# Kernel optimization log

Hardware: AMD Instinct MI355X
Metric: run time of the kernel (lower is better)

The kernel has to match this reference:

```python
import jax, jax.numpy as jnp
import numpy as np

C = 256
H_CH = 128  # channels // 2 (stage_index != 2)


def _gelu(x):
    # torch nn.GELU() default: exact erf formulation
    return jax.nn.gelu(x, approximate=False)


def _ln_channels(x, gamma, beta):
    # LayerNorm over channel dim (axis=1) of NCHW, eps=1e-5 (torch default)
    mu = jnp.mean(x, axis=1, keepdims=True)
    var = jnp.var(x, axis=1, keepdims=True)
    xn = (x - mu) * jax.lax.rsqrt(var + 1e-5)
    return xn * gamma[None, :, None, None] + beta[None, :, None, None]


def setup_inputs() -> dict:
    key = jax.random.key(0)
    ks = jax.random.split(key, 9)
    x = jax.random.normal(ks[0], (16, C, 64, 64), dtype=jnp.float32)
    s1 = 1.0 / np.sqrt(C)
    s2 = 1.0 / np.sqrt(H_CH)
    W1 = jax.random.uniform(ks[1], (H_CH, C), jnp.float32, -s1, s1)
    b1 = jax.random.uniform(ks[2], (H_CH,), jnp.float32, -s1, s1)
    g1 = jnp.ones((H_CH,), jnp.float32)
    be1 = jnp.zeros((H_CH,), jnp.float32)
    W2 = jax.random.uniform(ks[3], (C, H_CH), jnp.float32, -s2, s2)
    b2 = jax.random.uniform(ks[4], (C,), jnp.float32, -s2, s2)
    g2 = jnp.ones((C,), jnp.float32)
    be2 = jnp.zeros((C,), jnp.float32)
    return {"x": x, "W1": W1, "b1": b1, "g1": g1, "be1": be1,
            "W2": W2, "b2": b2, "g2": g2, "be2": be2}


def reference(x, W1, b1, g1, be1, W2, b2, g2, be2):
    identity = x
    # 1x1 conv == per-pixel channel matmul
    h = jnp.einsum('bchw,oc->bohw', x, W1) + b1[None, :, None, None]
    h = _gelu(_ln_channels(h, g1, be1))
    y = jnp.einsum('bchw,oc->bohw', h, W2) + b2[None, :, None, None]
    y = _ln_channels(y, g2, be2)
    return _gelu(y + identity)
```

## Files before the change

kernel.cpp:

```cpp
#include <hip/hip_runtime.h>

#define C_IN 256
#define HC   128
#define HW   4096
#define TP   64

#define SX 260
#define SH 132
#define SO 68

typedef __attribute__((ext_vector_type(8))) short short8;
typedef __attribute__((ext_vector_type(4))) short short4v;
typedef __attribute__((ext_vector_type(4))) float f32x4;
typedef __attribute__((ext_vector_type(2))) float f32x2;
typedef __attribute__((ext_vector_type(4))) unsigned short u16x4;

__device__ __forceinline__ unsigned short f2bf(float f) {
    union { float f; unsigned int u; } v; v.f = f;
    return (unsigned short)((v.u + 0x7FFFu + ((v.u >> 16) & 1u)) >> 16);
}

__device__ __forceinline__ float gelu_f(float v) {
    const float u = v * (0.7978845608028654f + 0.035677408136300125f * v * v);
    const float e = exp2f(u * 2.8853900817779268f);
    const float t = 1.0f - 2.0f * __builtin_amdgcn_rcpf(e + 1.0f);
    return 0.5f * v * (1.0f + t);
}

__device__ __forceinline__ void block_sync() {
    asm volatile("s_waitcnt lgkmcnt(0)" ::: "memory");
    __builtin_amdgcn_s_barrier();
    asm volatile("" ::: "memory");
    __builtin_amdgcn_sched_barrier(0);
}

__device__ __forceinline__ void wave_lds_fence() {
    asm volatile("s_waitcnt lgkmcnt(0)" ::: "memory");
}

__global__ void convert_weights(const float* __restrict__ W1, const float* __restrict__ W2,
                                unsigned short* __restrict__ W1b, unsigned short* __restrict__ W2b) {
    int i = blockIdx.x * blockDim.x + threadIdx.x;
    if (i < HC * C_IN) { W1b[i] = f2bf(W1[i]); W2b[i] = f2bf(W2[i]); }
}

union SmemU {
    unsigned short Xs[TP * SX];
    struct { unsigned short Hs[TP * SH]; float Ob[4][16][SO]; } u2;
};

template<bool USE_WS>
__global__ __launch_bounds__(256, 4) void fused_mlp(
    const float* __restrict__ x,
    const float* __restrict__ W1, const float* __restrict__ b1,
    const float* __restrict__ g1, const float* __restrict__ be1,
    const float* __restrict__ W2, const float* __restrict__ b2,
    const float* __restrict__ g2, const float* __restrict__ be2,
    const unsigned short* __restrict__ W1b, const unsigned short* __restrict__ W2b,
    float* __restrict__ out)
{
    __shared__ alignas(16) SmemU sm;
    __shared__ float red[4][TP][2];

    const int tid = threadIdx.x;
    const int wv  = tid >> 6;
    const int l   = tid & 63;
    const int l15 = l & 15;
    const int kg  = l >> 4;

    const int bid = blockIdx.x;
    const int b   = bid >> 6;
    const int p0  = (bid & 63) * TP;
    const float* xb = x   + (size_t)b * (C_IN * HW) + p0;
    float*       ob = out + (size_t)b * (C_IN * HW) + p0;

    const int g  = l15;
    const int cs = wv * 16 + kg * 4;
    f32x4 v0[8], v1[8];
    #pragma unroll
    for (int rnd = 0; rnd < 2; ++rnd)
        #pragma unroll
        for (int j = 0; j < 4; ++j)
            v0[rnd * 4 + j] = *reinterpret_cast<const f32x4*>(xb + (size_t)(rnd * 64 + cs + j) * HW + g * 4);
    #pragma unroll
    for (int rnd = 0; rnd < 2; ++rnd)
        #pragma unroll
        for (int j = 0; j < 4; ++j)
            v1[rnd * 4 + j] = *reinterpret_cast<const f32x4*>(xb + (size_t)((rnd + 2) * 64 + cs + j) * HW + g * 4);
    #pragma unroll
    for (int rnd = 0; rnd < 2; ++rnd) {
        const int c0 = rnd * 64 + cs;
        #pragma unroll
        for (int jj = 0; jj < 4; ++jj) {
            u16x4 pk;
            #pragma unroll
            for (int j = 0; j < 4; ++j) pk[j] = f2bf(v0[rnd * 4 + j][jj]);
            *reinterpret_cast<u16x4*>(&sm.Xs[(size_t)(g * 4 + jj) * SX + c0]) = pk;
        }
    }
    block_sync();

    f32x4 acc1[2][4];
    const f32x4 vzero = {0.f, 0.f, 0.f, 0.f};
    #pragma unroll
    for (int mt = 0; mt < 2; ++mt)
        #pragma unroll
        for (int nt = 0; nt < 4; ++nt) acc1[mt][nt] = vzero;

    const int r0 = wv * 32;
    #pragma unroll
    for (int ks = 0; ks < 4; ++ks) {
        const int kb = ks * 32 + kg * 8;
        short8 a[2]; short4v blo[4], bhi[4];
        #pragma unroll
        for (int mt = 0; mt < 2; ++mt) {
            const int row = r0 + mt * 16 + l15;
            if constexpr (USE_WS) {
                a[mt] = *reinterpret_cast<const short8*>(W1b + (size_t)row * C_IN + kb);
            } else {
                const float* wp = W1 + (size_t)row * C_IN + kb;
                const f32x4 f0 = *reinterpret_cast<const f32x4*>(wp);
                const f32x4 f1 = *reinterpret_cast<const f32x4*>(wp + 4);
                #pragma unroll
                for (int e = 0; e < 4; ++e) { a[mt][e] = (short)f2bf(f0[e]); a[mt][4+e] = (short)f2bf(f1[e]); }
            }
        }
        #pragma unroll
        for (int nt = 0; nt < 4; ++nt) {
            const unsigned short* p = &sm.Xs[(size_t)(nt * 16 + l15) * SX + kb];
            blo[nt] = *reinterpret_cast<const short4v*>(p);
            bhi[nt] = *reinterpret_cast<const short4v*>(p + 4);
        }
        #pragma unroll
        for (int mt = 0; mt < 2; ++mt)
            #pragma unroll
            for (int nt = 0; nt < 4; ++nt) {
                const short8 bf = __builtin_shufflevector(blo[nt], bhi[nt], 0,1,2,3,4,5,6,7);
                acc1[mt][nt] = __builtin_amdgcn_mfma_f32_16x16x32_bf16(a[mt], bf, acc1[mt][nt], 0, 0, 0);
            }
    }

    #pragma unroll
    for (int rnd = 0; rnd < 2; ++rnd) {
        const int c0 = (rnd + 2) * 64 + cs;
        #pragma unroll
        for (int jj = 0; jj < 4; ++jj) {
            u16x4 pk;
            #pragma unroll
            for (int j = 0; j < 4; ++j) pk[j] = f2bf(v1[rnd * 4 + j][jj]);
            *reinterpret_cast<u16x4*>(&sm.Xs[(size_t)(g * 4 + jj) * SX + c0]) = pk;
        }
    }
    block_sync();

    #pragma unroll
    for (int ks = 4; ks < 8; ++ks) {
        const int kb = ks * 32 + kg * 8;
        short8 a[2]; short4v blo[4], bhi[4];
        #pragma unroll
        for (int mt = 0; mt < 2; ++mt) {
            const int row = r0 + mt * 16 + l15;
            if constexpr (USE_WS) {
                a[mt] = *reinterpret_cast<const short8*>(W1b + (size_t)row * C_IN + kb);
            } else {
                const float* wp = W1 + (size_t)row * C_IN + kb;
                const f32x4 f0 = *reinterpret_cast<const f32x4*>(wp);
                const f32x4 f1 = *reinterpret_cast<const f32x4*>(wp + 4);
                #pragma unroll
                for (int e = 0; e < 4; ++e) { a[mt][e] = (short)f2bf(f0[e]); a[mt][4+e] = (short)f2bf(f1[e]); }
            }
        }
        #pragma unroll
        for (int nt = 0; nt < 4; ++nt) {
            const unsigned short* p = &sm.Xs[(size_t)(nt * 16 + l15) * SX + kb];
            blo[nt] = *reinterpret_cast<const short4v*>(p);
            bhi[nt] = *reinterpret_cast<const short4v*>(p + 4);
        }
        #pragma unroll
        for (int mt = 0; mt < 2; ++mt)
            #pragma unroll
            for (int nt = 0; nt < 4; ++nt) {
                const short8 bf = __builtin_shufflevector(blo[nt], bhi[nt], 0,1,2,3,4,5,6,7);
                acc1[mt][nt] = __builtin_amdgcn_mfma_f32_16x16x32_bf16(a[mt], bf, acc1[mt][nt], 0, 0, 0);
            }
    }

    #pragma unroll
    for (int mt = 0; mt < 2; ++mt) {
        const f32x4 bias = *reinterpret_cast<const f32x4*>(b1 + r0 + mt * 16 + kg * 4);
        #pragma unroll
        for (int nt = 0; nt < 4; ++nt) acc1[mt][nt] += bias;
    }
    #pragma unroll
    for (int nt = 0; nt < 4; ++nt) {
        float s = 0.f, q = 0.f;
        #pragma unroll
        for (int mt = 0; mt < 2; ++mt)
            #pragma unroll
            for (int r = 0; r < 4; ++r) { const float v = acc1[mt][nt][r]; s += v; q += v * v; }
        s += __shfl_xor(s, 16); s += __shfl_xor(s, 32);
        q += __shfl_xor(q, 16); q += __shfl_xor(q, 32);
        if (kg == 0) { red[wv][nt * 16 + l15][0] = s; red[wv][nt * 16 + l15][1] = q; }
    }
    block_sync();

    {
        f32x4 gm[2], bt[2];
        #pragma unroll
        for (int mt = 0; mt < 2; ++mt) {
            gm[mt] = *reinterpret_cast<const f32x4*>(g1  + r0 + mt * 16 + kg * 4);
            bt[mt] = *reinterpret_cast<const f32x4*>(be1 + r0 + mt * 16 + kg * 4);
        }
        #pragma unroll
        for (int nt = 0; nt < 4; ++nt) {
            const int col = nt * 16 + l15;
            float s = 0.f, q = 0.f;
            #pragma unroll
            for (int w2 = 0; w2 < 4; ++w2) { s += red[w2][col][0]; q += red[w2][col][1]; }
            const float mean = s * (1.0f / HC);
            const float rstd = rsqrtf(q * (1.0f / HC) - mean * mean + 1e-5f);
            #pragma unroll
            for (int mt = 0; mt < 2; ++mt) {
                u16x4 pk;
                #pragma unroll
                for (int r = 0; r < 4; ++r) {
                    float v = (acc1[mt][nt][r] - mean) * rstd;
                    v = v * gm[mt][r] + bt[mt][r];
                    pk[r] = f2bf(gelu_f(v));
                }
                *reinterpret_cast<u16x4*>(&sm.u2.Hs[(size_t)col * SH + r0 + mt * 16 + kg * 4]) = pk;
            }
        }
    }
    block_sync();

    const int r2 = wv * 64;
    f32x4 xp[4];
    #pragma unroll
    for (int m = 0; m < 4; ++m)
        xp[m] = *reinterpret_cast<const f32x4*>(xb + (size_t)(r2 + kg + 4 * m) * HW + l15 * 4);

    f32x4 acc2[4][4];
    #pragma unroll
    for (int mt = 0; mt < 4; ++mt)
        #pragma unroll
        for (int nt = 0; nt < 4; ++nt) acc2[mt][nt] = vzero;

    #pragma unroll
    for (int ks = 0; ks < 4; ++ks) {
        const int kb = ks * 32 + kg * 8;
        short4v blo[4], bhi[4];
        #pragma unroll
        for (int nt = 0; nt < 4; ++nt) {
            const unsigned short* p = &sm.u2.Hs[(size_t)(nt * 16 + l15) * SH + kb];
            blo[nt] = *reinterpret_cast<const short4v*>(p);
            bhi[nt] = *reinterpret_cast<const short4v*>(p + 4);
        }
        #pragma unroll
        for (int half = 0; half < 2; ++half) {
            short8 a[2];
            #pragma unroll
            for (int m2 = 0; m2 < 2; ++m2) {
                const int row = r2 + (half * 2 + m2) * 16 + l15;
                if constexpr (USE_WS) {
                    a[m2] = *reinterpret_cast<const short8*>(W2b + (size_t)row * HC + kb);
                } else {
                    const float* wp = W2 + (size_t)row * HC + kb;
                    const f32x4 f0 = *reinterpret_cast<const f32x4*>(wp);
                    const f32x4 f1 = *reinterpret_cast<const f32x4*>(wp + 4);
                    #pragma unroll
                    for (int e = 0; e < 4; ++e) { a[m2][e] = (short)f2bf(f0[e]); a[m2][4+e] = (short)f2bf(f1[e]); }
                }
            }
            #pragma unroll
            for (int m2 = 0; m2 < 2; ++m2)
                #pragma unroll
                for (int nt = 0; nt < 4; ++nt) {
                    const short8 bf = __builtin_shufflevector(blo[nt], bhi[nt], 0,1,2,3,4,5,6,7);
                    acc2[half * 2 + m2][nt] = __builtin_amdgcn_mfma_f32_16x16x32_bf16(a[m2], bf, acc2[half * 2 + m2][nt], 0, 0, 0);
                }
        }
    }

    #pragma unroll
    for (int mt = 0; mt < 4; ++mt) {
        const f32x4 bias = *reinterpret_cast<const f32x4*>(b2 + r2 + mt * 16 + kg * 4);
        #pragma unroll
        for (int nt = 0; nt < 4; ++nt) acc2[mt][nt] += bias;
    }
    #pragma unroll
    for (int nt = 0; nt < 4; ++nt) {
        float s = 0.f, q = 0.f;
        #pragma unroll
        for (int mt = 0; mt < 4; ++mt)
            #pragma unroll
            for (int r = 0; r < 4; ++r) { const float v = acc2[mt][nt][r]; s += v; q += v * v; }
        s += __shfl_xor(s, 16); s += __shfl_xor(s, 32);
        q += __shfl_xor(q, 16); q += __shfl_xor(q, 32);
        if (kg == 0) { red[wv][nt * 16 + l15][0] = s; red[wv][nt * 16 + l15][1] = q; }
    }
    block_sync();

    float mean2[4], rstd2[4];
    #pragma unroll
    for (int nt = 0; nt < 4; ++nt) {
        const int col = nt * 16 + l15;
        float s = 0.f, q = 0.f;
        #pragma unroll
        for (int w2 = 0; w2 < 4; ++w2) { s += red[w2][col][0]; q += red[w2][col][1]; }
        mean2[nt] = s * (1.0f / C_IN);
        rstd2[nt] = rsqrtf(q * (1.0f / C_IN) - mean2[nt] * mean2[nt] + 1e-5f);
    }

    #pragma unroll
    for (int mt = 0; mt < 4; ++mt) {
        const f32x4 gm = *reinterpret_cast<const f32x4*>(g2  + r2 + mt * 16 + kg * 4);
        const f32x4 bt = *reinterpret_cast<const f32x4*>(be2 + r2 + mt * 16 + kg * 4);
        #pragma unroll
        for (int nt = 0; nt < 4; ++nt) {
            #pragma unroll
            for (int r = 0; r < 4; ++r) {
                float v = (acc2[mt][nt][r] - mean2[nt]) * rstd2[nt];
                v = v * gm[r] + bt[r];
                sm.u2.Ob[wv][kg * 4 + r][nt * 16 + l15] = v;
            }
        }
        f32x4 xn[4];
        if (mt < 3) {
            #pragma unroll
            for (int m = 0; m < 4; ++m)
                xn[m] = *reinterpret_cast<const f32x4*>(xb + (size_t)(r2 + (mt + 1) * 16 + kg + 4 * m) * HW + l15 * 4);
        }
        wave_lds_fence();
        #pragma unroll
        for (int m = 0; m < 4; ++m) {
            const int rl  = kg + 4 * m;
            const int row = r2 + mt * 16 + rl;
            const float* op = &sm.u2.Ob[wv][rl][l15 * 4];
            const f32x2 ylo = *reinterpret_cast<const f32x2*>(op);
            const f32x2 yhi = *reinterpret_cast<const f32x2*>(op + 2);
            f32x4 o4;
            o4[0] = gelu_f(ylo[0] + xp[m][0]);
            o4[1] = gelu_f(ylo[1] + xp[m][1]);
            o4[2] = gelu_f(yhi[0] + xp[m][2]);
            o4[3] = gelu_f(yhi[1] + xp[m][3]);
            *reinterpret_cast<f32x4*>(ob + (size_t)row * HW + l15 * 4) = o4;
        }
        #pragma unroll
        for (int m = 0; m < 4; ++m) xp[m] = xn[m];
        if (mt < 3) wave_lds_fence();
    }
}

extern "C" void kernel_launch(void* const* d_in, const int* in_sizes, int n_in,
                              void* d_out, int out_size, void* d_ws, size_t ws_size,
                              hipStream_t stream) {
    const float* x   = (const float*)d_in[0];
    const float* W1  = (const float*)d_in[1];
    const float* b1  = (const float*)d_in[2];
    const float* g1  = (const float*)d_in[3];
    const float* be1 = (const float*)d_in[4];
    const float* W2  = (const float*)d_in[5];
    const float* b2  = (const float*)d_in[6];
    const float* g2  = (const float*)d_in[7];
    const float* be2 = (const float*)d_in[8];
    float* out = (float*)d_out;

    const size_t need = (size_t)(HC * C_IN + C_IN * HC) * sizeof(unsigned short);
    if (ws_size >= need) {
        unsigned short* W1b = (unsigned short*)d_ws;
        unsigned short* W2b = W1b + HC * C_IN;
        convert_weights<<<128, 256, 0, stream>>>(W1, W2, W1b, W2b);
        fused_mlp<true><<<1024, 256, 0, stream>>>(x, W1, b1, g1, be1, W2, b2, g2, be2, W1b, W2b, out);
    } else {
        fused_mlp<false><<<1024, 256, 0, stream>>>(x, W1, b1, g1, be1, W2, b2, g2, be2, nullptr, nullptr, out);
    }
}
```

Before: 57.97 us.

## Split X staging by pixel halves and overlap second-half conversion with GEMM1

The X tile is now loaded as two pixel halves instead of two channel halves, each spanning all 256 channels. The first GEMM runs over the full K on the first 32 pixels, and the bf16 conversion and LDS stores of the second 32 pixels are spread across its k-steps. The second pixel half is then processed over the full K. This is meant to hide the conversion and store work behind MFMA execution and to change the global load pattern to 128-byte pixel runs. In exchange, W1 A-fragments are loaded twice, once for each pixel half, and each k-step issues fewer MFMAs.

```diff
diff --git a/kernel.cpp b/kernel.cpp
--- a/kernel.cpp
+++ b/kernel.cpp
@@ -74,28 +74,30 @@
     const float* xb = x   + (size_t)b * (C_IN * HW) + p0;
     float*       ob = out + (size_t)b * (C_IN * HW) + p0;
 
-    const int g  = l15;
-    const int cs = wv * 16 + kg * 4;
-    f32x4 v0[8], v1[8];
+    const int gs = tid & 7;
+    const int cq = tid >> 3;
+
+    f32x4 vA[8], vB[8];
     #pragma unroll
     for (int rnd = 0; rnd < 2; ++rnd)
         #pragma unroll
         for (int j = 0; j < 4; ++j)
-            v0[rnd * 4 + j] = *reinterpret_cast<const f32x4*>(xb + (size_t)(rnd * 64 + cs + j) * HW + g * 4);
+            vA[rnd * 4 + j] = *reinterpret_cast<const f32x4*>(xb + (size_t)(rnd * 128 + cq * 4 + j) * HW + gs * 4);
     #pragma unroll
     for (int rnd = 0; rnd < 2; ++rnd)
         #pragma unroll
         for (int j = 0; j < 4; ++j)
-            v1[rnd * 4 + j] = *reinterpret_cast<const f32x4*>(xb + (size_t)((rnd + 2) * 64 + cs + j) * HW + g * 4);
+            vB[rnd * 4 + j] = *reinterpret_cast<const f32x4*>(xb + (size_t)(rnd * 128 + cq * 4 + j) * HW + 32 + gs * 4);
+
     #pragma unroll
     for (int rnd = 0; rnd < 2; ++rnd) {
-        const int c0 = rnd * 64 + cs;
+        const int c0 = rnd * 128 + cq * 4;
         #pragma unroll
         for (int jj = 0; jj < 4; ++jj) {
             u16x4 pk;
             #pragma unroll
-            for (int j = 0; j < 4; ++j) pk[j] = f2bf(v0[rnd * 4 + j][jj]);
-            *reinterpret_cast<u16x4*>(&sm.Xs[(size_t)(g * 4 + jj) * SX + c0]) = pk;
+            for (int j = 0; j < 4; ++j) pk[j] = f2bf(vA[rnd * 4 + j][jj]);
+            *reinterpret_cast<u16x4*>(&sm.Xs[(size_t)(gs * 4 + jj) * SX + c0]) = pk;
         }
     }
     block_sync();
@@ -109,9 +111,9 @@
 
     const int r0 = wv * 32;
     #pragma unroll
-    for (int ks = 0; ks < 4; ++ks) {
+    for (int ks = 0; ks < 8; ++ks) {
         const int kb = ks * 32 + kg * 8;
-        short8 a[2]; short4v blo[4], bhi[4];
+        short8 a[2]; short4v blo[2], bhi[2];
         #pragma unroll
         for (int mt = 0; mt < 2; ++mt) {
             const int row = r0 + mt * 16 + l15;
@@ -126,7 +128,7 @@
             }
         }
         #pragma unroll
-        for (int nt = 0; nt < 4; ++nt) {
+        for (int nt = 0; nt < 2; ++nt) {
             const unsigned short* p = &sm.Xs[(size_t)(nt * 16 + l15) * SX + kb];
             blo[nt] = *reinterpret_cast<const short4v*>(p);
             bhi[nt] = *reinterpret_cast<const short4v*>(p + 4);
@@ -134,29 +136,24 @@
         #pragma unroll
         for (int mt = 0; mt < 2; ++mt)
             #pragma unroll
-            for (int nt = 0; nt < 4; ++nt) {
+            for (int nt = 0; nt < 2; ++nt) {
                 const short8 bf = __builtin_shufflevector(blo[nt], bhi[nt], 0,1,2,3,4,5,6,7);
                 acc1[mt][nt] = __builtin_amdgcn_mfma_f32_16x16x32_bf16(a[mt], bf, acc1[mt][nt], 0, 0, 0);
             }
-    }
-
-    #pragma unroll
-    for (int rnd = 0; rnd < 2; ++rnd) {
-        const int c0 = (rnd + 2) * 64 + cs;
-        #pragma unroll
-        for (int jj = 0; jj < 4; ++jj) {
+        {
+            const int rnd = ks >> 2, jj = ks & 3;
             u16x4 pk;
             #pragma unroll
-            for (int j = 0; j < 4; ++j) pk[j] = f2bf(v1[rnd * 4 + j][jj]);
-            *reinterpret_cast<u16x4*>(&sm.Xs[(size_t)(g * 4 + jj) * SX + c0]) = pk;
-        }
-    }
-    block_sync();
-
-    #pragma unroll
-    for (int ks = 4; ks < 8; ++ks) {
+            for (int j = 0; j < 4; ++j) pk[j] = f2bf(vB[rnd * 4 + j][jj]);
+            *reinterpret_cast<u16x4*>(&sm.Xs[(size_t)(32 + gs * 4 + jj) * SX + rnd * 128 + cq * 4]) = pk;
+        }
+    }
+    block_sync();
+
+    #pragma unroll
+    for (int ks = 0; ks < 8; ++ks) {
         const int kb = ks * 32 + kg * 8;
-        short8 a[2]; short4v blo[4], bhi[4];
+        short8 a[2]; short4v blo[2], bhi[2];
         #pragma unroll
         for (int mt = 0; mt < 2; ++mt) {
             const int row = r0 + mt * 16 + l15;
@@ -171,17 +168,17 @@
             }
         }
         #pragma unroll
-        for (int nt = 0; nt < 4; ++nt) {
-            const unsigned short* p = &sm.Xs[(size_t)(nt * 16 + l15) * SX + kb];
+        for (int nt = 0; nt < 2; ++nt) {
+            const unsigned short* p = &sm.Xs[(size_t)((nt + 2) * 16 + l15) * SX + kb];
             blo[nt] = *reinterpret_cast<const short4v*>(p);
             bhi[nt] = *reinterpret_cast<const short4v*>(p + 4);
         }
         #pragma unroll
         for (int mt = 0; mt < 2; ++mt)
             #pragma unroll
-            for (int nt = 0; nt < 4; ++nt) {
+            for (int nt = 0; nt < 2; ++nt) {
                 const short8 bf = __builtin_shufflevector(blo[nt], bhi[nt], 0,1,2,3,4,5,6,7);
-                acc1[mt][nt] = __builtin_amdgcn_mfma_f32_16x16x32_bf16(a[mt], bf, acc1[mt][nt], 0, 0, 0);
+                acc1[mt][nt + 2] = __builtin_amdgcn_mfma_f32_16x16x32_bf16(a[mt], bf, acc1[mt][nt + 2], 0, 0, 0);
             }
     }
 
```

New measurement: 62.66 us. +8.1%, slower.

## Process two pixel tiles per block and prefetch the next tile's input during GEMM2

Applied to the files above, without the earlier changes.

Each block now handles two consecutive 64-pixel tiles, launching half as many blocks. The second tile's x data is loaded into registers after the first tile's LayerNorm-1, so the load overlaps GEMM2 and the epilogue. Shared memory is doubled to two buffers, and launch bounds drop to 2 blocks per CU. This targets exposed global load latency at the cost of lower occupancy, more register pressure, and fewer blocks to fill the GPU.

```diff
diff --git a/kernel.cpp b/kernel.cpp
--- a/kernel.cpp
+++ b/kernel.cpp
@@ -50,7 +50,7 @@
 };
 
 template<bool USE_WS>
-__global__ __launch_bounds__(256, 4) void fused_mlp(
+__global__ __launch_bounds__(256, 2) void fused_mlp(
     const float* __restrict__ x,
     const float* __restrict__ W1, const float* __restrict__ b1,
     const float* __restrict__ g1, const float* __restrict__ be1,
@@ -59,7 +59,7 @@
     const unsigned short* __restrict__ W1b, const unsigned short* __restrict__ W2b,
     float* __restrict__ out)
 {
-    __shared__ alignas(16) SmemU sm;
+    __shared__ alignas(16) SmemU sm[2];
     __shared__ float red[4][TP][2];
 
     const int tid = threadIdx.x;
@@ -68,287 +68,254 @@
     const int l15 = l & 15;
     const int kg  = l >> 4;
 
-    const int bid = blockIdx.x;
-    const int b   = bid >> 6;
-    const int p0  = (bid & 63) * TP;
-    const float* xb = x   + (size_t)b * (C_IN * HW) + p0;
-    float*       ob = out + (size_t)b * (C_IN * HW) + p0;
-
     const int g  = l15;
     const int cs = wv * 16 + kg * 4;
-    f32x4 v0[8], v1[8];
+
+    const int r0 = wv * 32;
+    const int r2 = wv * 64;
+    const f32x4 vzero = {0.f, 0.f, 0.f, 0.f};
+
+    const int tile0 = blockIdx.x * 2;
+    const float* xb0 = x + (size_t)(tile0 >> 6) * (C_IN * HW) + (tile0 & 63) * TP;
+    f32x4 vA[16];
     #pragma unroll
-    for (int rnd = 0; rnd < 2; ++rnd)
+    for (int rnd = 0; rnd < 4; ++rnd)
         #pragma unroll
         for (int j = 0; j < 4; ++j)
-            v0[rnd * 4 + j] = *reinterpret_cast<const f32x4*>(xb + (size_t)(rnd * 64 + cs + j) * HW + g * 4);
+            vA[rnd * 4 + j] = *reinterpret_cast<const f32x4*>(xb0 + (size_t)(rnd * 64 + cs + j) * HW + g * 4);
+
     #pragma unroll
-    for (int rnd = 0; rnd < 2; ++rnd)
-        #pragma unroll
-        for (int j = 0; j < 4; ++j)
-            v1[rnd * 4 + j] = *reinterpret_cast<const f32x4*>(xb + (size_t)((rnd + 2) * 64 + cs + j) * HW + g * 4);
-    #pragma unroll
-    for (int rnd = 0; rnd < 2; ++rnd) {
-        const int c0 = rnd * 64 + cs;
-        #pragma unroll
-        for (int jj = 0; jj < 4; ++jj) {
-            u16x4 pk;
-            #pragma unroll
-            for (int j = 0; j < 4; ++j) pk[j] = f2bf(v0[rnd * 4 + j][jj]);
-            *reinterpret_cast<u16x4*>(&sm.Xs[(size_t)(g * 4 + jj) * SX + c0]) = pk;
-        }
-    }
-    block_sync();
-
-    f32x4 acc1[2][4];
-    const f32x4 vzero = {0.f, 0.f, 0.f, 0.f};
-    #pragma unroll
-    for (int mt = 0; mt < 2; ++mt)
-        #pragma unroll
-        for (int nt = 0; nt < 4; ++nt) acc1[mt][nt] = vzero;
-
-    const int r0 = wv * 32;
-    #pragma unroll
-    for (int ks = 0; ks < 4; ++ks) {
-        const int kb = ks * 32 + kg * 8;
-        short8 a[2]; short4v blo[4], bhi[4];
+    for (int t = 0; t < 2; ++t) {
+        SmemU& S = sm[t];
+        const int tile = blockIdx.x * 2 + t;
+        const float* xb = x   + (size_t)(tile >> 6) * (C_IN * HW) + (tile & 63) * TP;
+        float*       ob = out + (size_t)(tile >> 6) * (C_IN * HW) + (tile & 63) * TP;
+
+        #pragma unroll
+        for (int rnd = 0; rnd < 4; ++rnd) {
+            const int c0 = rnd * 64 + cs;
+            #pragma unroll
+            for (int jj = 0; jj < 4; ++jj) {
+                u16x4 pk;
+                #pragma unroll
+                for (int j = 0; j < 4; ++j) pk[j] = f2bf(vA[rnd * 4 + j][jj]);
+                *reinterpret_cast<u16x4*>(&S.Xs[(size_t)(g * 4 + jj) * SX + c0]) = pk;
+            }
+        }
+        block_sync();
+
+        f32x4 acc1[2][4];
+        #pragma unroll
+        for (int mt = 0; mt < 2; ++mt)
+            #pragma unroll
+            for (int nt = 0; nt < 4; ++nt) acc1[mt][nt] = vzero;
+
+        #pragma unroll
+        for (int ks = 0; ks < 8; ++ks) {
+            const int kb = ks * 32 + kg * 8;
+            short8 a[2]; short4v blo[4], bhi[4];
+            #pragma unroll
+            for (int mt = 0; mt < 2; ++mt) {
+                const int row = r0 + mt * 16 + l15;
+                if constexpr (USE_WS) {
+                    a[mt] = *reinterpret_cast<const short8*>(W1b + (size_t)row * C_IN + kb);
+                } else {
+                    const float* wp = W1 + (size_t)row * C_IN + kb;
+                    const f32x4 f0 = *reinterpret_cast<const f32x4*>(wp);
+                    const f32x4 f1 = *reinterpret_cast<const f32x4*>(wp + 4);
+                    #pragma unroll
+                    for (int e = 0; e < 4; ++e) { a[mt][e] = (short)f2bf(f0[e]); a[mt][4+e] = (short)f2bf(f1[e]); }
+                }
+            }
+            #pragma unroll
+            for (int nt = 0; nt < 4; ++nt) {
+                const unsigned short* p = &S.Xs[(size_t)(nt * 16 + l15) * SX + kb];
+                blo[nt] = *reinterpret_cast<const short4v*>(p);
+                bhi[nt] = *reinterpret_cast<const short4v*>(p + 4);
+            }
+            #pragma unroll
+            for (int mt = 0; mt < 2; ++mt)
+                #pragma unroll
+                for (int nt = 0; nt < 4; ++nt) {
+                    const short8 bf = __builtin_shufflevector(blo[nt], bhi[nt], 0,1,2,3,4,5,6,7);
+                    acc1[mt][nt] = __builtin_amdgcn_mfma_f32_16x16x32_bf16(a[mt], bf, acc1[mt][nt], 0, 0, 0);
+                }
+        }
+
         #pragma unroll
         for (int mt = 0; mt < 2; ++mt) {
-            const int row = r0 + mt * 16 + l15;
-            if constexpr (USE_WS) {
-                a[mt] = *reinterpret_cast<const short8*>(W1b + (size_t)row * C_IN + kb);
-            } else {
-                const float* wp = W1 + (size_t)row * C_IN + kb;
-                const f32x4 f0 = *reinterpret_cast<const f32x4*>(wp);
-                const f32x4 f1 = *reinterpret_cast<const f32x4*>(wp + 4);
-                #pragma unroll
-                for (int e = 0; e < 4; ++e) { a[mt][e] = (short)f2bf(f0[e]); a[mt][4+e] = (short)f2bf(f1[e]); }
-            }
+            const f32x4 bias = *reinterpret_cast<const f32x4*>(b1 + r0 + mt * 16 + kg * 4);
+            #pragma unroll
+            for (int nt = 0; nt < 4; ++nt) acc1[mt][nt] += bias;
         }
         #pragma unroll
         for (int nt = 0; nt < 4; ++nt) {
-            const unsigned short* p = &sm.Xs[(size_t)(nt * 16 + l15) * SX + kb];
-            blo[nt] = *reinterpret_cast<const short4v*>(p);
-            bhi[nt] = *reinterpret_cast<const short4v*>(p + 4);
-        }
-        #pragma unroll
-        for (int mt = 0; mt < 2; ++mt)
+            float s = 0.f, q = 0.f;
+            #pragma unroll
+            for (int mt = 0; mt < 2; ++mt)
+                #pragma unroll
+                for (int r = 0; r < 4; ++r) { const float v = acc1[mt][nt][r]; s += v; q += v * v; }
+            s += __shfl_xor(s, 16); s += __shfl_xor(s, 32);
+            q += __shfl_xor(q, 16); q += __shfl_xor(q, 32);
+            if (kg == 0) { red[wv][nt * 16 + l15][0] = s; red[wv][nt * 16 + l15][1] = q; }
+        }
+        block_sync();
+
+        {
+            f32x4 gm[2], bt[2];
+            #pragma unroll
+            for (int mt = 0; mt < 2; ++mt) {
+                gm[mt] = *reinterpret_cast<const f32x4*>(g1  + r0 + mt * 16 + kg * 4);
+                bt[mt] = *reinterpret_cast<const f32x4*>(be1 + r0 + mt * 16 + kg * 4);
+            }
             #pragma unroll
             for (int nt = 0; nt < 4; ++nt) {
-                const short8 bf = __builtin_shufflevector(blo[nt], bhi[nt], 0,1,2,3,4,5,6,7);
-                acc1[mt][nt] = __builtin_amdgcn_mfma_f32_16x16x32_bf16(a[mt], bf, acc1[mt][nt], 0, 0, 0);
-            }
-    }
-
-    #pragma unroll
-    for (int rnd = 0; rnd < 2; ++rnd) {
-        const int c0 = (rnd + 2) * 64 + cs;
-        #pragma unroll
-        for (int jj = 0; jj < 4; ++jj) {
-            u16x4 pk;
-            #pragma unroll
-            for (int j = 0; j < 4; ++j) pk[j] = f2bf(v1[rnd * 4 + j][jj]);
-            *reinterpret_cast<u16x4*>(&sm.Xs[(size_t)(g * 4 + jj) * SX + c0]) = pk;
-        }
-    }
-    block_sync();
-
-    #pragma unroll
-    for (int ks = 4; ks < 8; ++ks) {
-        const int kb = ks * 32 + kg * 8;
-        short8 a[2]; short4v blo[4], bhi[4];
-        #pragma unroll
-        for (int mt = 0; mt < 2; ++mt) {
-            const int row = r0 + mt * 16 + l15;
-            if constexpr (USE_WS) {
-                a[mt] = *reinterpret_cast<const short8*>(W1b + (size_t)row * C_IN + kb);
-            } else {
-                const float* wp = W1 + (size_t)row * C_IN + kb;
-                const f32x4 f0 = *reinterpret_cast<const f32x4*>(wp);
-                const f32x4 f1 = *reinterpret_cast<const f32x4*>(wp + 4);
-                #pragma unroll
-                for (int e = 0; e < 4; ++e) { a[mt][e] = (short)f2bf(f0[e]); a[mt][4+e] = (short)f2bf(f1[e]); }
-            }
+                const int col = nt * 16 + l15;
+                float s = 0.f, q = 0.f;
+                #pragma unroll
+                for (int w2 = 0; w2 < 4; ++w2) { s += red[w2][col][0]; q += red[w2][col][1]; }
+                const float mean = s * (1.0f / HC);
+                const float rstd = rsqrtf(q * (1.0f / HC) - mean * mean + 1e-5f);
+                #pragma unroll
+                for (int mt = 0; mt < 2; ++mt) {
+                    u16x4 pk;
+                    #pragma unroll
+                    for (int r = 0; r < 4; ++r) {
+                        float v = (acc1[mt][nt][r] - mean) * rstd;
+                        v = v * gm[mt][r] + bt[mt][r];
+                        pk[r] = f2bf(gelu_f(v));
+                    }
+                    *reinterpret_cast<u16x4*>(&S.u2.Hs[(size_t)col * SH + r0 + mt * 16 + kg * 4]) = pk;
+                }
+            }
+        }
+        block_sync();
+
+        if (t == 0) {
+            const int tile1 = blockIdx.x * 2 + 1;
+            const float* xb1 = x + (size_t)(tile1 >> 6) * (C_IN * HW) + (tile1 & 63) * TP;
+            #pragma unroll
+            for (int rnd = 0; rnd < 4; ++rnd)
+                #pragma unroll
+                for (int j = 0; j < 4; ++j)
+                    vA[rnd * 4 + j] = *reinterpret_cast<const f32x4*>(xb1 + (size_t)(rnd * 64 + cs + j) * HW + g * 4);
+        }
+
+        f32x4 xp[4];
+        #pragma unroll
+        for (int m = 0; m < 4; ++m)
+            xp[m] = *reinterpret_cast<const f32x4*>(xb + (size_t)(r2 + kg + 4 * m) * HW + l15 * 4);
+
+        f32x4 acc2[4][4];
+        #pragma unroll
+        for (int mt = 0; mt < 4; ++mt)
+            #pragma unroll
+            for (int nt = 0; nt < 4; ++nt) acc2[mt][nt] = vzero;
+
+        #pragma unroll
+        for (int ks = 0; ks < 4; ++ks) {
+            const int kb = ks * 32 + kg * 8;
+            short4v blo[4], bhi[4];
+            #pragma unroll
+            for (int nt = 0; nt < 4; ++nt) {
+                const unsigned short* p = &S.u2.Hs[(size_t)(nt * 16 + l15) * SH + kb];
+                blo[nt] = *reinterpret_cast<const short4v*>(p);
+                bhi[nt] = *reinterpret_cast<const short4v*>(p + 4);
+            }
+            #pragma unroll
+            for (int half = 0; half < 2; ++half) {
+                short8 a[2];
+                #pragma unroll
+                for (int m2 = 0; m2 < 2; ++m2) {
+                    const int row = r2 + (half * 2 + m2) * 16 + l15;
+                    if constexpr (USE_WS) {
+                        a[m2] = *reinterpret_cast<const short8*>(W2b + (size_t)row * HC + kb);
+                    } else {
+                        const float* wp = W2 + (size_t)row * HC + kb;
+                        const f32x4 f0 = *reinterpret_cast<const f32x4*>(wp);
+                        const f32x4 f1 = *reinterpret_cast<const f32x4*>(wp + 4);
+                        #pragma unroll
+                        for (int e = 0; e < 4; ++e) { a[m2][e] = (short)f2bf(f0[e]); a[m2][4+e] = (short)f2bf(f1[e]); }
+                    }
+                }
+                #pragma unroll
+                for (int m2 = 0; m2 < 2; ++m2)
+                    #pragma unroll
+                    for (int nt = 0; nt < 4; ++nt) {
+                        const short8 bf = __builtin_shufflevector(blo[nt], bhi[nt], 0,1,2,3,4,5,6,7);
+                        acc2[half * 2 + m2][nt] = __builtin_amdgcn_mfma_f32_16x16x32_bf16(a[m2], bf, acc2[half * 2 + m2][nt], 0, 0, 0);
+                    }
+            }
+        }
+
+        #pragma unroll
+        for (int mt = 0; mt < 4; ++mt) {
+            const f32x4 bias = *reinterpret_cast<const f32x4*>(b2 + r2 + mt * 16 + kg * 4);
+            #pragma unroll
+            for (int nt = 0; nt < 4; ++nt) acc2[mt][nt] += bias;
         }
         #pragma unroll
         for (int nt = 0; nt < 4; ++nt) {
-            const unsigned short* p = &sm.Xs[(size_t)(nt * 16 + l15) * SX + kb];
-            blo[nt] = *reinterpret_cast<const short4v*>(p);
-            bhi[nt] = *reinterpret_cast<const short4v*>(p + 4);
-        }
-        #pragma unroll
-        for (int mt = 0; mt < 2; ++mt)
-            #pragma unroll
-            for (int nt = 0; nt < 4; ++nt) {
-                const short8 bf = __builtin_shufflevector(blo[nt], bhi[nt], 0,1,2,3,4,5,6,7);
-                acc1[mt][nt] = __builtin_amdgcn_mfma_f32_16x16x32_bf16(a[mt], bf, acc1[mt][nt], 0, 0, 0);
-            }
-    }
-
-    #pragma unroll
-    for (int mt = 0; mt < 2; ++mt) {
-        const f32x4 bias = *reinterpret_cast<const f32x4*>(b1 + r0 + mt * 16 + kg * 4);
-        #pragma unroll
-        for (int nt = 0; nt < 4; ++nt) acc1[mt][nt] += bias;
-    }
-    #pragma unroll
-    for (int nt = 0; nt < 4; ++nt) {
-        float s = 0.f, q = 0.f;
-        #pragma unroll
-        for (int mt = 0; mt < 2; ++mt)
-            #pragma unroll
-            for (int r = 0; r < 4; ++r) { const float v = acc1[mt][nt][r]; s += v; q += v * v; }
-        s += __shfl_xor(s, 16); s += __shfl_xor(s, 32);
-        q += __shfl_xor(q, 16); q += __shfl_xor(q, 32);
-        if (kg == 0) { red[wv][nt * 16 + l15][0] = s; red[wv][nt * 16 + l15][1] = q; }
-    }
-    block_sync();
-
-    {
-        f32x4 gm[2], bt[2];
-        #pragma unroll
-        for (int mt = 0; mt < 2; ++mt) {
-            gm[mt] = *reinterpret_cast<const f32x4*>(g1  + r0 + mt * 16 + kg * 4);
-            bt[mt] = *reinterpret_cast<const f32x4*>(be1 + r0 + mt * 16 + kg * 4);
-        }
+            float s = 0.f, q = 0.f;
+            #pragma unroll
+            for (int mt = 0; mt < 4; ++mt)
+                #pragma unroll
+                for (int r = 0; r < 4; ++r) { const float v = acc2[mt][nt][r]; s += v; q += v * v; }
+            s += __shfl_xor(s, 16); s += __shfl_xor(s, 32);
+            q += __shfl_xor(q, 16); q += __shfl_xor(q, 32);
+            if (kg == 0) { red[wv][nt * 16 + l15][0] = s; red[wv][nt * 16 + l15][1] = q; }
+        }
+        block_sync();
+
+        float mean2[4], rstd2[4];
         #pragma unroll
         for (int nt = 0; nt < 4; ++nt) {
             const int col = nt * 16 + l15;
             float s = 0.f, q = 0.f;
             #pragma unroll
             for (int w2 = 0; w2 < 4; ++w2) { s += red[w2][col][0]; q += red[w2][col][1]; }
-            const float mean = s * (1.0f / HC);
-            const float rstd = rsqrtf(q * (1.0f / HC) - mean * mean + 1e-5f);
-            #pragma unroll
-            for (int mt = 0; mt < 2; ++mt) {
-                u16x4 pk;
+            mean2[nt] = s * (1.0f / C_IN);
+            rstd2[nt] = rsqrtf(q * (1.0f / C_IN) - mean2[nt] * mean2[nt] + 1e-5f);
+        }
+
+        #pragma unroll
+        for (int mt = 0; mt < 4; ++mt) {
+            const f32x4 gm = *reinterpret_cast<const f32x4*>(g2  + r2 + mt * 16 + kg * 4);
+            const f32x4 bt = *reinterpret_cast<const f32x4*>(be2 + r2 + mt * 16 + kg * 4);
+            #pragma unroll
+            for (int nt = 0; nt < 4; ++nt) {
                 #pragma unroll
                 for (int r = 0; r < 4; ++r) {
-                    float v = (acc1[mt][nt][r] - mean) * rstd;
-                    v = v * gm[mt][r] + bt[mt][r];
-                    pk[r] = f2bf(gelu_f(v));
-                }
-                *reinterpret_cast<u16x4*>(&sm.u2.Hs[(size_t)col * SH + r0 + mt * 16 + kg * 4]) = pk;
-            }
-        }
-    }
-    block_sync();
-
-    const int r2 = wv * 64;
-    f32x4 xp[4];
-    #pragma unroll
-    for (int m = 0; m < 4; ++m)
-        xp[m] = *reinterpret_cast<const f32x4*>(xb + (size_t)(r2 + kg + 4 * m) * HW + l15 * 4);
-
-    f32x4 acc2[4][4];
-    #pragma unroll
-    for (int mt = 0; mt < 4; ++mt)
-        #pragma unroll
-        for (int nt = 0; nt < 4; ++nt) acc2[mt][nt] = vzero;
-
-    #pragma unroll
-    for (int ks = 0; ks < 4; ++ks) {
-        const int kb = ks * 32 + kg * 8;
-        short4v blo[4], bhi[4];
-        #pragma unroll
-        for (int nt = 0; nt < 4; ++nt) {
-            const unsigned short* p = &sm.u2.Hs[(size_t)(nt * 16 + l15) * SH + kb];
-            blo[nt] = *reinterpret_cast<const short4v*>(p);
-            bhi[nt] = *reinterpret_cast<const short4v*>(p + 4);
-        }
-        #pragma unroll
-        for (int half = 0; half < 2; ++half) {
-            short8 a[2];
-            #pragma unroll
-            for (int m2 = 0; m2 < 2; ++m2) {
-                const int row = r2 + (half * 2 + m2) * 16 + l15;
-                if constexpr (USE_WS) {
-                    a[m2] = *reinterpret_cast<const short8*>(W2b + (size_t)row * HC + kb);
-                } else {
-                    const float* wp = W2 + (size_t)row * HC + kb;
-                    const f32x4 f0 = *reinterpret_cast<const f32x4*>(wp);
-                    const f32x4 f1 = *reinterpret_cast<const f32x4*>(wp + 4);
-                    #pragma unroll
-                    for (int e = 0; e < 4; ++e) { a[m2][e] = (short)f2bf(f0[e]); a[m2][4+e] = (short)f2bf(f1[e]); }
-                }
-            }
-            #pragma unroll
-            for (int m2 = 0; m2 < 2; ++m2)
-                #pragma unroll
-                for (int nt = 0; nt < 4; ++nt) {
-                    const short8 bf = __builtin_shufflevector(blo[nt], bhi[nt], 0,1,2,3,4,5,6,7);
-                    acc2[half * 2 + m2][nt] = __builtin_amdgcn_mfma_f32_16x16x32_bf16(a[m2], bf, acc2[half * 2 + m2][nt], 0, 0, 0);
-                }
-        }
-    }
-
-    #pragma unroll
-    for (int mt = 0; mt < 4; ++mt) {
-        const f32x4 bias = *reinterpret_cast<const f32x4*>(b2 + r2 + mt * 16 + kg * 4);
-        #pragma unroll
-        for (int nt = 0; nt < 4; ++nt) acc2[mt][nt] += bias;
-    }
-    #pragma unroll
-    for (int nt = 0; nt < 4; ++nt) {
-        float s = 0.f, q = 0.f;
-        #pragma unroll
-        for (int mt = 0; mt < 4; ++mt)
-            #pragma unroll
-            for (int r = 0; r < 4; ++r) { const float v = acc2[mt][nt][r]; s += v; q += v * v; }
-        s += __shfl_xor(s, 16); s += __shfl_xor(s, 32);
-        q += __shfl_xor(q, 16); q += __shfl_xor(q, 32);
-        if (kg == 0) { red[wv][nt * 16 + l15][0] = s; red[wv][nt * 16 + l15][1] = q; }
-    }
-    block_sync();
-
-    float mean2[4], rstd2[4];
-    #pragma unroll
-    for (int nt = 0; nt < 4; ++nt) {
-        const int col = nt * 16 + l15;
-        float s = 0.f, q = 0.f;
-        #pragma unroll
-        for (int w2 = 0; w2 < 4; ++w2) { s += red[w2][col][0]; q += red[w2][col][1]; }
-        mean2[nt] = s * (1.0f / C_IN);
-        rstd2[nt] = rsqrtf(q * (1.0f / C_IN) - mean2[nt] * mean2[nt] + 1e-5f);
-    }
-
-    #pragma unroll
-    for (int mt = 0; mt < 4; ++mt) {
-        const f32x4 gm = *reinterpret_cast<const f32x4*>(g2  + r2 + mt * 16 + kg * 4);
-        const f32x4 bt = *reinterpret_cast<const f32x4*>(be2 + r2 + mt * 16 + kg * 4);
-        #pragma unroll
-        for (int nt = 0; nt < 4; ++nt) {
-            #pragma unroll
-            for (int r = 0; r < 4; ++r) {
-                float v = (acc2[mt][nt][r] - mean2[nt]) * rstd2[nt];
-                v = v * gm[r] + bt[r];
-                sm.u2.Ob[wv][kg * 4 + r][nt * 16 + l15] = v;
-            }
-        }
-        f32x4 xn[4];
-        if (mt < 3) {
-            #pragma unroll
-            for (int m = 0; m < 4; ++m)
-                xn[m] = *reinterpret_cast<const f32x4*>(xb + (size_t)(r2 + (mt + 1) * 16 + kg + 4 * m) * HW + l15 * 4);
-        }
-        wave_lds_fence();
-        #pragma unroll
-        for (int m = 0; m < 4; ++m) {
-            const int rl  = kg + 4 * m;
-            const int row = r2 + mt * 16 + rl;
-            const float* op = &sm.u2.Ob[wv][rl][l15 * 4];
-            const f32x2 ylo = *reinterpret_cast<const f32x2*>(op);
-            const f32x2 yhi = *reinterpret_cast<const f32x2*>(op + 2);
-            f32x4 o4;
-            o4[0] = gelu_f(ylo[0] + xp[m][0]);
-            o4[1] = gelu_f(ylo[1] + xp[m][1]);
-            o4[2] = gelu_f(yhi[0] + xp[m][2]);
-            o4[3] = gelu_f(yhi[1] + xp[m][3]);
-            *reinterpret_cast<f32x4*>(ob + (size_t)row * HW + l15 * 4) = o4;
-        }
-        #pragma unroll
-        for (int m = 0; m < 4; ++m) xp[m] = xn[m];
-        if (mt < 3) wave_lds_fence();
+                    float v = (acc2[mt][nt][r] - mean2[nt]) * rstd2[nt];
+                    v = v * gm[r] + bt[r];
+                    S.u2.Ob[wv][kg * 4 + r][nt * 16 + l15] = v;
+                }
+            }
+            f32x4 xn[4];
+            if (mt < 3) {
+                #pragma unroll
+                for (int m = 0; m < 4; ++m)
+                    xn[m] = *reinterpret_cast<const f32x4*>(xb + (size_t)(r2 + (mt + 1) * 16 + kg + 4 * m) * HW + l15 * 4);
+            }
+            wave_lds_fence();
+            #pragma unroll
+            for (int m = 0; m < 4; ++m) {
+                const int rl  = kg + 4 * m;
+                const int row = r2 + mt * 16 + rl;
+                const float* op = &S.u2.Ob[wv][rl][l15 * 4];
+                const f32x2 ylo = *reinterpret_cast<const f32x2*>(op);
+                const f32x2 yhi = *reinterpret_cast<const f32x2*>(op + 2);
+                f32x4 o4;
+                o4[0] = gelu_f(ylo[0] + xp[m][0]);
+                o4[1] = gelu_f(ylo[1] + xp[m][1]);
+                o4[2] = gelu_f(yhi[0] + xp[m][2]);
+                o4[3] = gelu_f(yhi[1] + xp[m][3]);
+                *reinterpret_cast<f32x4*>(ob + (size_t)row * HW + l15 * 4) = o4;
+            }
+            #pragma unroll
+            for (int m = 0; m < 4; ++m) xp[m] = xn[m];
+            if (mt < 3) wave_lds_fence();
+        }
     }
 }
 
@@ -371,8 +338,8 @@
         unsigned short* W1b = (unsigned short*)d_ws;
         unsigned short* W2b = W1b + HC * C_IN;
         convert_weights<<<128, 256, 0, stream>>>(W1, W2, W1b, W2b);
-        fused_mlp<true><<<1024, 256, 0, stream>>>(x, W1, b1, g1, be1, W2, b2, g2, be2, W1b, W2b, out);
+        fused_mlp<true><<<512, 256, 0, stream>>>(x, W1, b1, g1, be1, W2, b2, g2, be2, W1b, W2b, out);
     } else {
-        fused_mlp<false><<<1024, 256, 0, stream>>>(x, W1, b1, g1, be1, W2, b2, g2, be2, nullptr, nullptr, out);
+        fused_mlp<false><<<512, 256, 0, stream>>>(x, W1, b1, g1, be1, W2, b2, g2, be2, nullptr, nullptr, out);
     }
 }
```

New measurement: 64.17 us. +10.7%, slower.

## Split fused MLP into two kernels with bf16 hidden activations in workspace

Applied to the files above, without the earlier changes.

Adds a two-kernel path: one kernel runs the first GEMM with LayerNorm and GELU and writes the hidden activations as bf16 to global workspace, and a second kernel reads them to run the second GEMM, LayerNorm, residual add and GELU. This runs whenever the workspace is large enough for the hidden buffer, and is meant to cut per-kernel LDS and register pressure and improve occupancy. In exchange it adds a 16 MB bf16 write and read round trip through global memory, reads x twice, and adds an extra launch.

```diff
diff --git a/kernel.cpp b/kernel.cpp
--- a/kernel.cpp
+++ b/kernel.cpp
@@ -6,7 +6,6 @@
 #define TP   64
 
 #define SX 260
-#define SH 132
 #define SO 68
 
 typedef __attribute__((ext_vector_type(8))) short short8;
@@ -15,6 +14,8 @@
 typedef __attribute__((ext_vector_type(2))) float f32x2;
 typedef __attribute__((ext_vector_type(4))) unsigned short u16x4;
 
+#define SH 132
+
 __device__ __forceinline__ unsigned short f2bf(float f) {
     union { float f; unsigned int u; } v; v.f = f;
     return (unsigned short)((v.u + 0x7FFFu + ((v.u >> 16) & 1u)) >> 16);
@@ -42,6 +43,251 @@
                                 unsigned short* __restrict__ W1b, unsigned short* __restrict__ W2b) {
     int i = blockIdx.x * blockDim.x + threadIdx.x;
     if (i < HC * C_IN) { W1b[i] = f2bf(W1[i]); W2b[i] = f2bf(W2[i]); }
+}
+
+__global__ __launch_bounds__(256, 4) void gemm1_ln(
+    const float* __restrict__ x, const float* __restrict__ b1,
+    const float* __restrict__ g1, const float* __restrict__ be1,
+    const unsigned short* __restrict__ W1b, unsigned short* __restrict__ H)
+{
+    __shared__ alignas(16) unsigned short Xs[TP * SX];
+    __shared__ float red[4][TP][2];
+
+    const int tid = threadIdx.x;
+    const int wv  = tid >> 6;
+    const int l   = tid & 63;
+    const int l15 = l & 15;
+    const int kg  = l >> 4;
+
+    const int bid = blockIdx.x;
+    const int b   = bid >> 6;
+    const int p0  = (bid & 63) * TP;
+    const float* xb = x + (size_t)b * (C_IN * HW) + p0;
+
+    const int g  = l15;
+    const int cs = wv * 16 + kg * 4;
+    f32x4 vA[16];
+    #pragma unroll
+    for (int rnd = 0; rnd < 4; ++rnd)
+        #pragma unroll
+        for (int j = 0; j < 4; ++j)
+            vA[rnd * 4 + j] = *reinterpret_cast<const f32x4*>(xb + (size_t)(rnd * 64 + cs + j) * HW + g * 4);
+    #pragma unroll
+    for (int rnd = 0; rnd < 4; ++rnd) {
+        const int c0 = rnd * 64 + cs;
+        #pragma unroll
+        for (int jj = 0; jj < 4; ++jj) {
+            u16x4 pk;
+            #pragma unroll
+            for (int j = 0; j < 4; ++j) pk[j] = f2bf(vA[rnd * 4 + j][jj]);
+            *reinterpret_cast<u16x4*>(&Xs[(size_t)(g * 4 + jj) * SX + c0]) = pk;
+        }
+    }
+    block_sync();
+
+    f32x4 acc1[2][4];
+    const f32x4 vzero = {0.f, 0.f, 0.f, 0.f};
+    #pragma unroll
+    for (int mt = 0; mt < 2; ++mt)
+        #pragma unroll
+        for (int nt = 0; nt < 4; ++nt) acc1[mt][nt] = vzero;
+
+    const int r0 = wv * 32;
+    #pragma unroll
+    for (int ks = 0; ks < 8; ++ks) {
+        const int kb = ks * 32 + kg * 8;
+        short8 a[2]; short4v blo[4], bhi[4];
+        #pragma unroll
+        for (int mt = 0; mt < 2; ++mt)
+            a[mt] = *reinterpret_cast<const short8*>(W1b + (size_t)(r0 + mt * 16 + l15) * C_IN + kb);
+        #pragma unroll
+        for (int nt = 0; nt < 4; ++nt) {
+            const unsigned short* p = &Xs[(size_t)(nt * 16 + l15) * SX + kb];
+            blo[nt] = *reinterpret_cast<const short4v*>(p);
+            bhi[nt] = *reinterpret_cast<const short4v*>(p + 4);
+        }
+        #pragma unroll
+        for (int mt = 0; mt < 2; ++mt)
+            #pragma unroll
+            for (int nt = 0; nt < 4; ++nt) {
+                const short8 bf = __builtin_shufflevector(blo[nt], bhi[nt], 0,1,2,3,4,5,6,7);
+                acc1[mt][nt] = __builtin_amdgcn_mfma_f32_16x16x32_bf16(a[mt], bf, acc1[mt][nt], 0, 0, 0);
+            }
+    }
+
+    #pragma unroll
+    for (int mt = 0; mt < 2; ++mt) {
+        const f32x4 bias = *reinterpret_cast<const f32x4*>(b1 + r0 + mt * 16 + kg * 4);
+        #pragma unroll
+        for (int nt = 0; nt < 4; ++nt) acc1[mt][nt] += bias;
+    }
+    #pragma unroll
+    for (int nt = 0; nt < 4; ++nt) {
+        float s = 0.f, q = 0.f;
+        #pragma unroll
+        for (int mt = 0; mt < 2; ++mt)
+            #pragma unroll
+            for (int r = 0; r < 4; ++r) { const float v = acc1[mt][nt][r]; s += v; q += v * v; }
+        s += __shfl_xor(s, 16); s += __shfl_xor(s, 32);
+        q += __shfl_xor(q, 16); q += __shfl_xor(q, 32);
+        if (kg == 0) { red[wv][nt * 16 + l15][0] = s; red[wv][nt * 16 + l15][1] = q; }
+    }
+    block_sync();
+
+    unsigned short* Hb = H + ((size_t)b * HW + p0) * HC;
+    f32x4 gm[2], bt[2];
+    #pragma unroll
+    for (int mt = 0; mt < 2; ++mt) {
+        gm[mt] = *reinterpret_cast<const f32x4*>(g1  + r0 + mt * 16 + kg * 4);
+        bt[mt] = *reinterpret_cast<const f32x4*>(be1 + r0 + mt * 16 + kg * 4);
+    }
+    #pragma unroll
+    for (int nt = 0; nt < 4; ++nt) {
+        const int col = nt * 16 + l15;
+        float s = 0.f, q = 0.f;
+        #pragma unroll
+        for (int w2 = 0; w2 < 4; ++w2) { s += red[w2][col][0]; q += red[w2][col][1]; }
+        const float mean = s * (1.0f / HC);
+        const float rstd = rsqrtf(q * (1.0f / HC) - mean * mean + 1e-5f);
+        #pragma unroll
+        for (int mt = 0; mt < 2; ++mt) {
+            u16x4 pk;
+            #pragma unroll
+            for (int r = 0; r < 4; ++r) {
+                float v = (acc1[mt][nt][r] - mean) * rstd;
+                v = v * gm[mt][r] + bt[mt][r];
+                pk[r] = f2bf(gelu_f(v));
+            }
+            *reinterpret_cast<u16x4*>(Hb + (size_t)col * HC + r0 + mt * 16 + kg * 4) = pk;
+        }
+    }
+}
+
+__global__ __launch_bounds__(256, 4) void gemm2_ln(
+    const float* __restrict__ x,
+    const float* __restrict__ b2, const float* __restrict__ g2, const float* __restrict__ be2,
+    const unsigned short* __restrict__ W2b, const unsigned short* __restrict__ H,
+    float* __restrict__ out)
+{
+    __shared__ alignas(16) float Ob[4][16][SO];
+    __shared__ float red[4][TP][2];
+
+    const int tid = threadIdx.x;
+    const int wv  = tid >> 6;
+    const int l   = tid & 63;
+    const int l15 = l & 15;
+    const int kg  = l >> 4;
+
+    const int bid = blockIdx.x;
+    const int b   = bid >> 6;
+    const int p0  = (bid & 63) * TP;
+    const float* xb = x   + (size_t)b * (C_IN * HW) + p0;
+    float*       ob = out + (size_t)b * (C_IN * HW) + p0;
+    const unsigned short* Hb = H + ((size_t)b * HW + p0) * HC;
+
+    const int r2 = wv * 64;
+    const f32x4 vzero = {0.f, 0.f, 0.f, 0.f};
+
+    f32x4 xp[4];
+    #pragma unroll
+    for (int m = 0; m < 4; ++m)
+        xp[m] = *reinterpret_cast<const f32x4*>(xb + (size_t)(r2 + kg + 4 * m) * HW + l15 * 4);
+
+    f32x4 acc2[4][4];
+    #pragma unroll
+    for (int mt = 0; mt < 4; ++mt)
+        #pragma unroll
+        for (int nt = 0; nt < 4; ++nt) acc2[mt][nt] = vzero;
+
+    #pragma unroll
+    for (int ks = 0; ks < 4; ++ks) {
+        const int kb = ks * 32 + kg * 8;
+        short8 bfr[4];
+        #pragma unroll
+        for (int nt = 0; nt < 4; ++nt)
+            bfr[nt] = *reinterpret_cast<const short8*>(Hb + (size_t)(nt * 16 + l15) * HC + kb);
+        #pragma unroll
+        for (int half = 0; half < 2; ++half) {
+            short8 a[2];
+            #pragma unroll
+            for (int m2 = 0; m2 < 2; ++m2)
+                a[m2] = *reinterpret_cast<const short8*>(W2b + (size_t)(r2 + (half * 2 + m2) * 16 + l15) * HC + kb);
+            #pragma unroll
+            for (int m2 = 0; m2 < 2; ++m2)
+                #pragma unroll
+                for (int nt = 0; nt < 4; ++nt)
+                    acc2[half * 2 + m2][nt] = __builtin_amdgcn_mfma_f32_16x16x32_bf16(a[m2], bfr[nt], acc2[half * 2 + m2][nt], 0, 0, 0);
+        }
+    }
+
+    #pragma unroll
+    for (int mt = 0; mt < 4; ++mt) {
+        const f32x4 bias = *reinterpret_cast<const f32x4*>(b2 + r2 + mt * 16 + kg * 4);
+        #pragma unroll
+        for (int nt = 0; nt < 4; ++nt) acc2[mt][nt] += bias;
+    }
+    #pragma unroll
+    for (int nt = 0; nt < 4; ++nt) {
+        float s = 0.f, q = 0.f;
+        #pragma unroll
+        for (int mt = 0; mt < 4; ++mt)
+            #pragma unroll
+            for (int r = 0; r < 4; ++r) { const float v = acc2[mt][nt][r]; s += v; q += v * v; }
+        s += __shfl_xor(s, 16); s += __shfl_xor(s, 32);
+        q += __shfl_xor(q, 16); q += __shfl_xor(q, 32);
+        if (kg == 0) { red[wv][nt * 16 + l15][0] = s; red[wv][nt * 16 + l15][1] = q; }
+    }
+    block_sync();
+
+    float mean2[4], rstd2[4];
+    #pragma unroll
+    for (int nt = 0; nt < 4; ++nt) {
+        const int col = nt * 16 + l15;
+        float s = 0.f, q = 0.f;
+        #pragma unroll
+        for (int w2 = 0; w2 < 4; ++w2) { s += red[w2][col][0]; q += red[w2][col][1]; }
+        mean2[nt] = s * (1.0f / C_IN);
+        rstd2[nt] = rsqrtf(q * (1.0f / C_IN) - mean2[nt] * mean2[nt] + 1e-5f);
+    }
+
+    #pragma unroll
+    for (int mt = 0; mt < 4; ++mt) {
+        const f32x4 gm = *reinterpret_cast<const f32x4*>(g2  + r2 + mt * 16 + kg * 4);
+        const f32x4 bt = *reinterpret_cast<const f32x4*>(be2 + r2 + mt * 16 + kg * 4);
+        #pragma unroll
+        for (int nt = 0; nt < 4; ++nt) {
+            #pragma unroll
+            for (int r = 0; r < 4; ++r) {
+                float v = (acc2[mt][nt][r] - mean2[nt]) * rstd2[nt];
+                v = v * gm[r] + bt[r];
+                Ob[wv][kg * 4 + r][nt * 16 + l15] = v;
+            }
+        }
+        f32x4 xn[4];
+        if (mt < 3) {
+            #pragma unroll
+            for (int m = 0; m < 4; ++m)
+                xn[m] = *reinterpret_cast<const f32x4*>(xb + (size_t)(r2 + (mt + 1) * 16 + kg + 4 * m) * HW + l15 * 4);
+        }
+        wave_lds_fence();
+        #pragma unroll
+        for (int m = 0; m < 4; ++m) {
+            const int rl  = kg + 4 * m;
+            const int row = r2 + mt * 16 + rl;
+            const float* op = &Ob[wv][rl][l15 * 4];
+            const f32x2 ylo = *reinterpret_cast<const f32x2*>(op);
+            const f32x2 yhi = *reinterpret_cast<const f32x2*>(op + 2);
+            f32x4 o4;
+            o4[0] = gelu_f(ylo[0] + xp[m][0]);
+            o4[1] = gelu_f(ylo[1] + xp[m][1]);
+            o4[2] = gelu_f(yhi[0] + xp[m][2]);
+            o4[3] = gelu_f(yhi[1] + xp[m][3]);
+            *reinterpret_cast<f32x4*>(ob + (size_t)row * HW + l15 * 4) = o4;
+        }
+        #pragma unroll
+        for (int m = 0; m < 4; ++m) xp[m] = xn[m];
+        if (mt < 3) wave_lds_fence();
+    }
 }
 
 union SmemU {
@@ -139,7 +385,6 @@
                 acc1[mt][nt] = __builtin_amdgcn_mfma_f32_16x16x32_bf16(a[mt], bf, acc1[mt][nt], 0, 0, 0);
             }
     }
-
     #pragma unroll
     for (int rnd = 0; rnd < 2; ++rnd) {
         const int c0 = (rnd + 2) * 64 + cs;
@@ -366,10 +611,17 @@
     const float* be2 = (const float*)d_in[8];
     float* out = (float*)d_out;
 
-    const size_t need = (size_t)(HC * C_IN + C_IN * HC) * sizeof(unsigned short);
-    if (ws_size >= need) {
-        unsigned short* W1b = (unsigned short*)d_ws;
-        unsigned short* W2b = W1b + HC * C_IN;
+    const size_t w_need = (size_t)(HC * C_IN + C_IN * HC) * sizeof(unsigned short);
+    const size_t h_need = (size_t)16 * HW * HC * sizeof(unsigned short);
+    unsigned short* W1b = (unsigned short*)d_ws;
+    unsigned short* W2b = W1b + HC * C_IN;
+    unsigned short* Hws = W2b + C_IN * HC;
+
+    if (ws_size >= w_need + h_need) {
+        convert_weights<<<128, 256, 0, stream>>>(W1, W2, W1b, W2b);
+        gemm1_ln<<<1024, 256, 0, stream>>>(x, b1, g1, be1, W1b, Hws);
+        gemm2_ln<<<1024, 256, 0, stream>>>(x, b2, g2, be2, W2b, Hws, out);
+    } else if (ws_size >= w_need) {
         convert_weights<<<128, 256, 0, stream>>>(W1, W2, W1b, W2b);
         fused_mlp<true><<<1024, 256, 0, stream>>>(x, W1, b1, g1, be1, W2, b2, g2, be2, W1b, W2b, out);
     } else {
```

Measured after the change: 72.59 us. +25.2%, slower.
